# Kernel tuning notes

Measured on AMD Instinct MI355X. Metric: run time of the kernel, lower is better.

The kernel has to match this reference:

```python
import jax, jax.numpy as jnp
import numpy as np

B, D_IN, D_Z, D_H, D_T, D_REC = 8192, 1024, 256, 256, 16, 256


def _softplus_beta(x, beta):
    # torch F.softplus(x, beta) = (1/beta) * log(1 + exp(beta*x))
    return jax.nn.softplus(beta * x) / beta


def setup_inputs() -> dict:
    key = jax.random.key(0)
    ks = jax.random.split(key, 17)
    w = lambda k, o, i: jax.random.normal(k, (o, i), jnp.float32) * (1.0 / np.sqrt(i))
    return {
        "I_t": jax.random.uniform(ks[0], (B, D_IN), jnp.float32),
        "h_m_1": jax.random.uniform(ks[1], (B, D_H), jnp.float32),
        "z_m_1": jax.random.uniform(ks[2], (B, D_Z), jnp.float32),
        "theta_m_1": jax.random.normal(ks[3], (B, D_T), jnp.float32),
        "eps_z": jax.random.normal(ks[4], (B, D_Z), jnp.float32),
        "eps_zhat": jax.random.normal(ks[5], (B, D_Z), jnp.float32),
        "W_post_mu": w(ks[6], D_Z, D_IN),
        "W_post_lv": w(ks[7], D_Z, D_IN),
        "W_z2h": w(ks[8], D_H, D_Z),
        "W_h2h": w(ks[9], D_H, D_H),
        "W_prior_mu": w(ks[10], D_Z, D_H),
        "W_prior_lv": w(ks[11], D_Z, D_H),
        "W_i2t": w(ks[12], D_T, D_IN),
        "W_vip2t": w(ks[13], D_T, D_Z),
        "W_t2z": w(ks[14], D_Z, D_T),
        "W_rec1": w(ks[15], D_REC, D_Z),
        "W_rec2": w(ks[16], D_IN, D_REC),
    }


def reference(I_t, h_m_1, z_m_1, theta_m_1, eps_z, eps_zhat,
              W_post_mu, W_post_lv, W_z2h, W_h2h, W_prior_mu, W_prior_lv,
              W_i2t, W_vip2t, W_t2z, W_rec1, W_rec2):
    relu = jax.nn.relu
    # prior pathway (perception_only=True branch)
    mu_p = relu(h_m_1 @ W_prior_mu.T)                       # [B, D_Z]
    sigma_p = _softplus_beta(h_m_1 @ W_prior_lv.T, 1.2)     # [B, D_Z]
    # theta dynamics; vip_to_theta has Positive parametrization -> relu(W)
    theta_h = (0.5 * theta_m_1 + 0.1 * (I_t @ W_i2t.T)
               - jax.lax.stop_gradient(sigma_p) @ relu(W_vip2t).T)  # [B, D_T]
    theta = 0.001 * _softplus_beta(theta_h, 0.5)
    # posterior + reparameterized sample
    mu_q = relu(I_t @ W_post_mu.T)
    sigma_q = relu(I_t @ W_post_lv.T)
    raw_z = jnp.clip(mu_q + eps_z * sigma_q, 0.0, 1.0)
    thresholds = 10.0 * (theta @ relu(W_t2z).T)             # Positive parametrization
    z = relu(raw_z - thresholds)                            # [B, D_Z]
    # reconstruction (two bias-free linears + sigmoid)
    I_hat = jax.nn.sigmoid((z @ W_rec1.T) @ W_rec2.T)       # [B, D_IN]
    # higher-state update and prior sample
    h = relu(z_m_1 @ W_z2h.T + h_m_1 @ W_h2h.T)             # [B, D_H]
    z_hat = mu_p + eps_zhat * sigma_p                       # [B, D_Z]
    # losses (as in torch forward)
    spatial = jnp.mean((I_t - I_hat) ** 2)
    temporal = jnp.mean((jax.lax.stop_gradient(z) - z_hat) ** 2)
    energy = jnp.mean(jnp.abs(z))
    return (I_hat, z, h, z_hat, spatial, temporal, energy)
```

## Files before the change

### kernel.cpp

```cpp
#include <hip/hip_runtime.h>
#include <math.h>

#define BB 8192
#define DIN 1024
#define DZ 256
#define DH 256
#define DT 16
#define DREC 256

#define OFF_IHAT 0
#define OFF_Z    (BB * DIN)
#define OFF_H    (OFF_Z + BB * DZ)
#define OFF_ZHAT (OFF_H + BB * DH)
#define OFF_SCAL (OFF_ZHAT + BB * DZ)

#define WS_HBF   0
#define WS_ZM1   2097152
#define WS_W     4194304
#define W_PM  (WS_W + 0)
#define W_PL  (W_PM + 262144)
#define W_Z2H (W_PL + 262144)
#define W_H2H (W_Z2H + 65536)
#define W_PRM (W_H2H + 65536)
#define W_PRL (W_PRM + 65536)
#define W_I2T (W_PRL + 65536)
#define W_VIP (W_I2T + 16384)
#define W_R1  (W_VIP + 4096)
#define W_R2  (W_R1 + 65536)
#define WS_ENDW  (W_R2 + 262144)
#define WS_SIGMA WS_ENDW
#define WS_ZBF   (WS_SIGMA + 2097152)
#define WS_R1BF  (WS_ZBF + 2097152)

typedef unsigned short u16;
typedef __attribute__((ext_vector_type(8))) unsigned short u16x8;
typedef __attribute__((ext_vector_type(8))) __bf16 bf16x8;
typedef __attribute__((ext_vector_type(4))) float f32x4;

#define MFMA __builtin_amdgcn_mfma_f32_16x16x32_bf16

__device__ inline u16 f2bf(float f) {
  unsigned u = __builtin_bit_cast(unsigned, f);
  u += 0x7fff + ((u >> 16) & 1);
  return (u16)(u >> 16);
}
__device__ inline float softplus_stable(float y) {
  return (y > 20.f) ? y : log1pf(expf(y));
}
__device__ inline bf16x8 gf(const u16* p) {
  return __builtin_bit_cast(bf16x8, *(const u16x8*)p);
}
__device__ inline f32x4 fzero() { return (f32x4){0.f, 0.f, 0.f, 0.f}; }

__device__ inline float block_sum256(float v, float* rbuf) {
#pragma unroll
  for (int off = 32; off > 0; off >>= 1) v += __shfl_down(v, off, 64);
  __syncthreads();
  if ((threadIdx.x & 63) == 0) rbuf[threadIdx.x >> 6] = v;
  __syncthreads();
  return rbuf[0] + rbuf[1] + rbuf[2] + rbuf[3];
}

__device__ inline void dma64(u16* tile, const u16* __restrict__ gsrc,
                             int row0, int ldk, int k0) {
  const int lane = threadIdx.x & 63, w = threadIdx.x >> 6;
#pragma unroll
  for (int c = 0; c < 2; ++c) {
    int rb = w * 16 + c * 8;
    int r = rb + (lane >> 3);
    int gl = (lane & 7) ^ (r & 7);
    const u16* src = gsrc + (size_t)(row0 + r) * ldk + k0 + gl * 8;
    u16* dst = tile + rb * 64;
    __builtin_amdgcn_global_load_lds(
        (const __attribute__((address_space(1))) unsigned int*)(const void*)src,
        (__attribute__((address_space(3))) unsigned int*)(void*)dst, 16, 0, 0);
  }
}
__device__ inline void dma16(u16* tile, const u16* __restrict__ gsrc,
                             int ldk, int k0) {
  const int lane = threadIdx.x & 63, w = threadIdx.x >> 6;
  if (w < 2) {
    int rb = w * 8;
    int r = rb + (lane >> 3);
    int gl = (lane & 7) ^ (r & 7);
    const u16* src = gsrc + (size_t)r * ldk + k0 + gl * 8;
    u16* dst = tile + rb * 64;
    __builtin_amdgcn_global_load_lds(
        (const __attribute__((address_space(1))) unsigned int*)(const void*)src,
        (__attribute__((address_space(3))) unsigned int*)(void*)dst, 16, 0, 0);
  }
}
__device__ inline bf16x8 rd(const u16* tile, int r, int gl) {
  return gf(tile + r * 64 + ((gl ^ (r & 7)) * 8));
}

__global__ __launch_bounds__(256) void k_cvt(
    const float* __restrict__ I_t, const float* __restrict__ h_m_1,
    const float* __restrict__ z_m_1, const float* __restrict__ Wpm,
    const float* __restrict__ Wpl, const float* __restrict__ Wz2h,
    const float* __restrict__ Wh2h, const float* __restrict__ Wprm,
    const float* __restrict__ Wprl, const float* __restrict__ Wi2t,
    const float* __restrict__ Wv, const float* __restrict__ Wr1,
    const float* __restrict__ Wr2, u16* __restrict__ dstI,
    u16* __restrict__ dstW) {
  const int S1 = 8388608, S2 = 10485760, S3 = 12582912, S4 = 12845056,
            S5 = 13107200, S6 = 13172736, S7 = 13238272, S8 = 13303808,
            S9 = 13369344, S10 = 13385728, S11 = 13389824, S12 = 13455360,
            S13 = 13717504;
  int nchunk = S13 / 8;
  for (int c = blockIdx.x * 256 + threadIdx.x; c < nchunk;
       c += gridDim.x * 256) {
    int f = c * 8;
    const float* src;
    float scale = 1.f;
    bool nrelu = false;
    u16* dst;
    if (f < S1) {
      src = I_t + f;
      dst = dstI + f;
    } else {
      dst = dstW + (f - S1);
      if (f < S2)       src = h_m_1 + (f - S1);
      else if (f < S3)  src = z_m_1 + (f - S2);
      else if (f < S4)  src = Wpm + (f - S3);
      else if (f < S5)  src = Wpl + (f - S4);
      else if (f < S6)  src = Wz2h + (f - S5);
      else if (f < S7)  src = Wh2h + (f - S6);
      else if (f < S8)  src = Wprm + (f - S7);
      else if (f < S9)  src = Wprl + (f - S8);
      else if (f < S10) { src = Wi2t + (f - S9);  scale = 0.1f; }
      else if (f < S11) { src = Wv + (f - S10);   nrelu = true; }
      else if (f < S12) src = Wr1 + (f - S11);
      else              src = Wr2 + (f - S12);
    }
    float4 v0 = *(const float4*)(src);
    float4 v1 = *(const float4*)(src + 4);
    float vals[8] = {v0.x, v0.y, v0.z, v0.w, v1.x, v1.y, v1.z, v1.w};
    u16x8 o;
#pragma unroll
    for (int j = 0; j < 8; ++j) {
      float x = vals[j];
      x = nrelu ? -fmaxf(x, 0.f) : x * scale;
      o[j] = f2bf(x);
    }
    *(u16x8*)(dst) = o;
  }
}

__global__ __launch_bounds__(256, 4) void k_hp(
    const u16* __restrict__ h_bf, const u16* __restrict__ zm1,
    const u16* __restrict__ Wh2h, const u16* __restrict__ Wprm,
    const u16* __restrict__ Wprl, const u16* __restrict__ Wz2h,
    const float* __restrict__ eps_zhat, float* __restrict__ h_out,
    float* __restrict__ zhat_out, u16* __restrict__ sigma_bf) {
  __shared__ __align__(16) u16 As[64 * 64], B0s[64 * 64], B1s[64 * 64],
      B2s[64 * 64];
  const int tid = threadIdx.x, lane = tid & 63, w = tid >> 6;
  const int frow = lane & 15, fq = lane >> 4;
  const int col0 = blockIdx.x * 64, row0 = blockIdx.y * 64;
  f32x4 ah[4], am[4], as_[4];
#pragma unroll
  for (int i = 0; i < 4; ++i) { ah[i] = fzero(); am[i] = fzero(); as_[i] = fzero(); }

  for (int k0 = 0; k0 < DH; k0 += 64) {
    __syncthreads();
    dma64(As, h_bf, row0, DH, k0);
    dma64(B0s, Wh2h, col0, DH, k0);
    dma64(B1s, Wprm, col0, DH, k0);
    dma64(B2s, Wprl, col0, DH, k0);
    __syncthreads();
#pragma unroll
    for (int ks = 0; ks < 2; ++ks) {
      bf16x8 a = rd(As, w * 16 + frow, ks * 4 + fq);
#pragma unroll
      for (int ni = 0; ni < 4; ++ni) {
        ah[ni]  = MFMA(a, rd(B0s, ni * 16 + frow, ks * 4 + fq), ah[ni], 0, 0, 0);
        am[ni]  = MFMA(a, rd(B1s, ni * 16 + frow, ks * 4 + fq), am[ni], 0, 0, 0);
        as_[ni] = MFMA(a, rd(B2s, ni * 16 + frow, ks * 4 + fq), as_[ni], 0, 0, 0);
      }
    }
  }
  for (int k0 = 0; k0 < DZ; k0 += 64) {
    __syncthreads();
    dma64(As, zm1, row0, DZ, k0);
    dma64(B0s, Wz2h, col0, DZ, k0);
    __syncthreads();
#pragma unroll
    for (int ks = 0; ks < 2; ++ks) {
      bf16x8 a = rd(As, w * 16 + frow, ks * 4 + fq);
#pragma unroll
      for (int ni = 0; ni < 4; ++ni)
        ah[ni] = MFMA(a, rd(B0s, ni * 16 + frow, ks * 4 + fq), ah[ni], 0, 0, 0);
    }
  }
#pragma unroll
  for (int ni = 0; ni < 4; ++ni)
#pragma unroll
    for (int r = 0; r < 4; ++r) {
      int m = row0 + w * 16 + fq * 4 + r;
      int n = col0 + ni * 16 + frow;
      h_out[(size_t)m * DH + n] = fmaxf(ah[ni][r], 0.f);
      float sig = softplus_stable(1.2f * as_[ni][r]) * (1.f / 1.2f);
      float mu = fmaxf(am[ni][r], 0.f);
      zhat_out[(size_t)m * DZ + n] = mu + eps_zhat[(size_t)m * DZ + n] * sig;
      sigma_bf[(size_t)m * DZ + n] = f2bf(sig);
    }
}

__global__ __launch_bounds__(256, 4) void k_post(
    const u16* __restrict__ I_bf, const u16* __restrict__ Wpm,
    const u16* __restrict__ Wpl, const u16* __restrict__ Wi2t,
    const u16* __restrict__ Wv, const u16* __restrict__ sigma_bf,
    const float* __restrict__ theta_m_1, const float* __restrict__ W_t2z,
    const float* __restrict__ eps_z, const float* __restrict__ zhat,
    float* __restrict__ z_out, u16* __restrict__ z_bf,
    float* __restrict__ scal) {
  __shared__ __align__(16) u16 As[64 * 64], B0s[64 * 64], B1s[64 * 64],
      Bts[16 * 64];
  __shared__ float th_s[64 * 17];
  __shared__ float wt_s[64 * 17];
  __shared__ float rbuf[4];
  const int tid = threadIdx.x, lane = tid & 63, w = tid >> 6;
  const int frow = lane & 15, fq = lane >> 4;
  const int col0 = blockIdx.x * 64, row0 = blockIdx.y * 64;
  f32x4 accm[4], accs[4], acct = fzero();
#pragma unroll
  for (int i = 0; i < 4; ++i) { accm[i] = fzero(); accs[i] = fzero(); }

  for (int k0 = 0; k0 < DIN; k0 += 64) {
    __syncthreads();
    dma64(As, I_bf, row0, DIN, k0);
    dma64(B0s, Wpm, col0, DIN, k0);
    dma64(B1s, Wpl, col0, DIN, k0);
    dma16(Bts, Wi2t, DIN, k0);
    __syncthreads();
#pragma unroll
    for (int ks = 0; ks < 2; ++ks) {
      bf16x8 a = rd(As, w * 16 + frow, ks * 4 + fq);
#pragma unroll
      for (int ni = 0; ni < 4; ++ni) {
        accm[ni] = MFMA(a, rd(B0s, ni * 16 + frow, ks * 4 + fq), accm[ni], 0, 0, 0);
        accs[ni] = MFMA(a, rd(B1s, ni * 16 + frow, ks * 4 + fq), accs[ni], 0, 0, 0);
      }
      acct = MFMA(a, rd(Bts, frow, ks * 4 + fq), acct, 0, 0, 0);
    }
  }
  for (int k0 = 0; k0 < DZ; k0 += 64) {
    __syncthreads();
    dma64(As, sigma_bf, row0, DZ, k0);
    dma16(Bts, Wv, DZ, k0);
    __syncthreads();
#pragma unroll
    for (int ks = 0; ks < 2; ++ks)
      acct = MFMA(rd(As, w * 16 + frow, ks * 4 + fq),
                  rd(Bts, frow, ks * 4 + fq), acct, 0, 0, 0);
  }
  __syncthreads();
#pragma unroll
  for (int r = 0; r < 4; ++r) {
    int lr = w * 16 + fq * 4 + r;
    float th = 0.5f * theta_m_1[(size_t)(row0 + lr) * DT + frow] + acct[r];
    th_s[lr * 17 + frow] = 0.002f * softplus_stable(0.5f * th);
  }
  for (int idx = tid; idx < 64 * 16; idx += 256) {
    int n = idx >> 4, j = idx & 15;
    wt_s[n * 17 + j] = 10.f * fmaxf(W_t2z[(col0 + n) * DT + j], 0.f);
  }
  __syncthreads();
  float tsum = 0.f, esum = 0.f;
#pragma unroll
  for (int ni = 0; ni < 4; ++ni)
#pragma unroll
    for (int r = 0; r < 4; ++r) {
      int lr = w * 16 + fq * 4 + r;
      int ln = ni * 16 + frow;
      int m = row0 + lr;
      int n = col0 + ln;
      float mu = fmaxf(accm[ni][r], 0.f);
      float sq = fmaxf(accs[ni][r], 0.f);
      float raw = mu + eps_z[(size_t)m * DZ + n] * sq;
      raw = fminf(fmaxf(raw, 0.f), 1.f);
      float thr = 0.f;
#pragma unroll
      for (int j = 0; j < 16; ++j)
        thr = fmaf(th_s[lr * 17 + j], wt_s[ln * 17 + j], thr);
      float zz = fmaxf(raw - thr, 0.f);
      z_out[(size_t)m * DZ + n] = zz;
      z_bf[(size_t)m * DZ + n] = f2bf(zz);
      float d = zz - zhat[(size_t)m * DZ + n];
      tsum += d * d;
      esum += zz;
    }
  float t = block_sum256(tsum, rbuf);
  if (tid == 0) atomicAdd(scal + 1, t * (1.f / ((float)BB * DZ)));
  float e = block_sum256(esum, rbuf);
  if (tid == 0) atomicAdd(scal + 2, e * (1.f / ((float)BB * DZ)));
}

__global__ __launch_bounds__(256, 4) void k_rec1(const u16* __restrict__ z_bf,
                                                 const u16* __restrict__ Wr1,
                                                 u16* __restrict__ r1_bf) {
  __shared__ __align__(16) u16 As[64 * 64], B0s[64 * 64];
  const int tid = threadIdx.x, lane = tid & 63, w = tid >> 6;
  const int frow = lane & 15, fq = lane >> 4;
  const int col0 = blockIdx.x * 64, row0 = blockIdx.y * 64;
  f32x4 acc[4] = {fzero(), fzero(), fzero(), fzero()};
  for (int k0 = 0; k0 < DZ; k0 += 64) {
    __syncthreads();
    dma64(As, z_bf, row0, DZ, k0);
    dma64(B0s, Wr1, col0, DZ, k0);
    __syncthreads();
#pragma unroll
    for (int ks = 0; ks < 2; ++ks) {
      bf16x8 a = rd(As, w * 16 + frow, ks * 4 + fq);
#pragma unroll
      for (int ni = 0; ni < 4; ++ni)
        acc[ni] = MFMA(a, rd(B0s, ni * 16 + frow, ks * 4 + fq), acc[ni], 0, 0, 0);
    }
  }
#pragma unroll
  for (int ni = 0; ni < 4; ++ni)
#pragma unroll
    for (int r = 0; r < 4; ++r) {
      int m = row0 + w * 16 + fq * 4 + r;
      int n = col0 + ni * 16 + frow;
      r1_bf[(size_t)m * DREC + n] = f2bf(acc[ni][r]);
    }
}

__global__ __launch_bounds__(256, 4) void k_rec2(const u16* __restrict__ r1_bf,
                                                 const u16* __restrict__ Wr2,
                                                 const float* __restrict__ I_t,
                                                 float* __restrict__ ihat_out,
                                                 float* __restrict__ scal) {
  __shared__ __align__(16) u16 As[64 * 64], B0s[64 * 64];
  __shared__ float rbuf[4];
  const int tid = threadIdx.x, lane = tid & 63, w = tid >> 6;
  const int frow = lane & 15, fq = lane >> 4;
  const int col0 = blockIdx.x * 64, row0 = blockIdx.y * 64;
  f32x4 acc[4] = {fzero(), fzero(), fzero(), fzero()};
  for (int k0 = 0; k0 < DREC; k0 += 64) {
    __syncthreads();
    dma64(As, r1_bf, row0, DREC, k0);
    dma64(B0s, Wr2, col0, DREC, k0);
    __syncthreads();
#pragma unroll
    for (int ks = 0; ks < 2; ++ks) {
      bf16x8 a = rd(As, w * 16 + frow, ks * 4 + fq);
#pragma unroll
      for (int ni = 0; ni < 4; ++ni)
        acc[ni] = MFMA(a, rd(B0s, ni * 16 + frow, ks * 4 + fq), acc[ni], 0, 0, 0);
    }
  }
  float lsum = 0.f;
#pragma unroll
  for (int ni = 0; ni < 4; ++ni)
#pragma unroll
    for (int r = 0; r < 4; ++r) {
      int m = row0 + w * 16 + fq * 4 + r;
      int n = col0 + ni * 16 + frow;
      float ih = 1.f / (1.f + expf(-acc[ni][r]));
      ihat_out[(size_t)m * DIN + n] = ih;
      float d = I_t[(size_t)m * DIN + n] - ih;
      lsum += d * d;
    }
  float s = block_sum256(lsum, rbuf);
  if (tid == 0) atomicAdd(scal + 0, s * (1.f / ((float)BB * DIN)));
}

extern "C" void kernel_launch(void* const* d_in, const int* in_sizes, int n_in,
                              void* d_out, int out_size, void* d_ws,
                              size_t ws_size, hipStream_t stream) {
  const float* I_t       = (const float*)d_in[0];
  const float* h_m_1     = (const float*)d_in[1];
  const float* z_m_1     = (const float*)d_in[2];
  const float* theta_m_1 = (const float*)d_in[3];
  const float* eps_z     = (const float*)d_in[4];
  const float* eps_zhat  = (const float*)d_in[5];
  const float* W_post_mu = (const float*)d_in[6];
  const float* W_post_lv = (const float*)d_in[7];
  const float* W_z2h     = (const float*)d_in[8];
  const float* W_h2h     = (const float*)d_in[9];
  const float* W_prior_mu= (const float*)d_in[10];
  const float* W_prior_lv= (const float*)d_in[11];
  const float* W_i2t     = (const float*)d_in[12];
  const float* W_vip2t   = (const float*)d_in[13];
  const float* W_t2z     = (const float*)d_in[14];
  const float* W_rec1    = (const float*)d_in[15];
  const float* W_rec2    = (const float*)d_in[16];

  float* out = (float*)d_out;
  float* ihat = out + OFF_IHAT;
  float* zout = out + OFF_Z;
  float* hout = out + OFF_H;
  float* zhat = out + OFF_ZHAT;
  float* scal = out + OFF_SCAL;

  u16* ws_u = (u16*)d_ws;
  u16* I_bf = (u16*)ihat;
  u16* h_bf = ws_u + WS_HBF;
  u16* zm1_bf = ws_u + WS_ZM1;
  u16* sigma_bf = ws_u + WS_SIGMA;
  u16* z_bf = ws_u + WS_ZBF;
  u16* r1_bf = ws_u + WS_R1BF;

  hipMemsetAsync(scal, 0, 3 * sizeof(float), stream);

  k_cvt<<<2048, 256, 0, stream>>>(I_t, h_m_1, z_m_1, W_post_mu, W_post_lv,
                                  W_z2h, W_h2h, W_prior_mu, W_prior_lv, W_i2t,
                                  W_vip2t, W_rec1, W_rec2, I_bf, ws_u + WS_HBF);

  dim3 gz(DZ / 64, BB / 64);
  dim3 gi(DIN / 64, BB / 64);

  k_hp<<<gz, 256, 0, stream>>>(h_bf, zm1_bf, ws_u + W_H2H, ws_u + W_PRM,
                               ws_u + W_PRL, ws_u + W_Z2H, eps_zhat, hout,
                               zhat, sigma_bf);
  k_post<<<gz, 256, 0, stream>>>(I_bf, ws_u + W_PM, ws_u + W_PL, ws_u + W_I2T,
                                 ws_u + W_VIP, sigma_bf, theta_m_1, W_t2z,
                                 eps_z, zhat, zout, z_bf, scal);
  k_rec1<<<gz, 256, 0, stream>>>(z_bf, ws_u + W_R1, r1_bf);
  k_rec2<<<gi, 256, 0, stream>>>(r1_bf, ws_u + W_R2, I_t, ihat, scal);
}
```

Before: 273.7 us.

## Shrink row tiles, swizzle blocks across XCDs, and stage epilogues through LDS

The three DZ-wide GEMM kernels now use 32x64 tiles on a 1D grid of 1024 blocks, giving twice as many blocks and a 2x2 wave layout. Block IDs are remapped so consecutive XCDs take adjacent row blocks that share weight columns. All epilogues now write results to padded LDS and then emit coalesced float4 and u16x8 global stores and loads, replacing scattered per-element accesses. The trade-off is extra LDS round trips and barriers, plus less MFMA work per A-fragment load in the smaller tiles.

```diff
diff --git a/kernel.cpp b/kernel.cpp
--- a/kernel.cpp
+++ b/kernel.cpp
@@ -61,8 +61,26 @@
   return rbuf[0] + rbuf[1] + rbuf[2] + rbuf[3];
 }
 
-__device__ inline void dma64(u16* tile, const u16* __restrict__ gsrc,
-                             int row0, int ldk, int k0) {
+__device__ inline void decode4(int id, int rows, int& row0, int& col0) {
+  int xcd = id & 7, t = id >> 3;
+  col0 = (t & 3) * 64;
+  row0 = ((t >> 2) * 8 + xcd) * rows;
+}
+
+__device__ inline void dmaA32(u16* tile, const u16* __restrict__ gsrc,
+                              int row0, int ldk, int k0) {
+  const int lane = threadIdx.x & 63, w = threadIdx.x >> 6;
+  int rb = w * 8;
+  int r = rb + (lane >> 3);
+  int gl = (lane & 7) ^ (r & 7);
+  const u16* src = gsrc + (size_t)(row0 + r) * ldk + k0 + gl * 8;
+  u16* dst = tile + rb * 64;
+  __builtin_amdgcn_global_load_lds(
+      (const __attribute__((address_space(1))) unsigned int*)(const void*)src,
+      (__attribute__((address_space(3))) unsigned int*)(void*)dst, 16, 0, 0);
+}
+__device__ inline void dmaB64(u16* tile, const u16* __restrict__ gsrc,
+                              int row0, int ldk, int k0) {
   const int lane = threadIdx.x & 63, w = threadIdx.x >> 6;
 #pragma unroll
   for (int c = 0; c < 2; ++c) {
@@ -76,8 +94,8 @@
         (__attribute__((address_space(3))) unsigned int*)(void*)dst, 16, 0, 0);
   }
 }
-__device__ inline void dma16(u16* tile, const u16* __restrict__ gsrc,
-                             int ldk, int k0) {
+__device__ inline void dma16(u16* tile, const u16* __restrict__ gsrc, int ldk,
+                             int k0) {
   const int lane = threadIdx.x & 63, w = threadIdx.x >> 6;
   if (w < 2) {
     int rb = w * 8;
@@ -153,58 +171,97 @@
     const u16* __restrict__ Wprl, const u16* __restrict__ Wz2h,
     const float* __restrict__ eps_zhat, float* __restrict__ h_out,
     float* __restrict__ zhat_out, u16* __restrict__ sigma_bf) {
-  __shared__ __align__(16) u16 As[64 * 64], B0s[64 * 64], B1s[64 * 64],
-      B2s[64 * 64];
+  __shared__ __align__(16) u16 smem[2048 + 3 * 4096];
+  u16* As = smem;
+  u16* B0s = smem + 2048;
+  u16* B1s = B0s + 4096;
+  u16* B2s = B1s + 4096;
   const int tid = threadIdx.x, lane = tid & 63, w = tid >> 6;
   const int frow = lane & 15, fq = lane >> 4;
-  const int col0 = blockIdx.x * 64, row0 = blockIdx.y * 64;
-  f32x4 ah[4], am[4], as_[4];
-#pragma unroll
-  for (int i = 0; i < 4; ++i) { ah[i] = fzero(); am[i] = fzero(); as_[i] = fzero(); }
+  const int wr = w & 1, wc = w >> 1;
+  int row0, col0;
+  decode4(blockIdx.x, 32, row0, col0);
+
+  f32x4 ah[2], am[2], as_[2];
+#pragma unroll
+  for (int i = 0; i < 2; ++i) { ah[i] = fzero(); am[i] = fzero(); as_[i] = fzero(); }
 
   for (int k0 = 0; k0 < DH; k0 += 64) {
     __syncthreads();
-    dma64(As, h_bf, row0, DH, k0);
-    dma64(B0s, Wh2h, col0, DH, k0);
-    dma64(B1s, Wprm, col0, DH, k0);
-    dma64(B2s, Wprl, col0, DH, k0);
+    dmaA32(As, h_bf, row0, DH, k0);
+    dmaB64(B0s, Wh2h, col0, DH, k0);
+    dmaB64(B1s, Wprm, col0, DH, k0);
+    dmaB64(B2s, Wprl, col0, DH, k0);
     __syncthreads();
 #pragma unroll
     for (int ks = 0; ks < 2; ++ks) {
-      bf16x8 a = rd(As, w * 16 + frow, ks * 4 + fq);
-#pragma unroll
-      for (int ni = 0; ni < 4; ++ni) {
-        ah[ni]  = MFMA(a, rd(B0s, ni * 16 + frow, ks * 4 + fq), ah[ni], 0, 0, 0);
-        am[ni]  = MFMA(a, rd(B1s, ni * 16 + frow, ks * 4 + fq), am[ni], 0, 0, 0);
-        as_[ni] = MFMA(a, rd(B2s, ni * 16 + frow, ks * 4 + fq), as_[ni], 0, 0, 0);
+      bf16x8 a = rd(As, wr * 16 + frow, ks * 4 + fq);
+#pragma unroll
+      for (int ni = 0; ni < 2; ++ni) {
+        int br = wc * 32 + ni * 16 + frow;
+        ah[ni]  = MFMA(a, rd(B0s, br, ks * 4 + fq), ah[ni], 0, 0, 0);
+        am[ni]  = MFMA(a, rd(B1s, br, ks * 4 + fq), am[ni], 0, 0, 0);
+        as_[ni] = MFMA(a, rd(B2s, br, ks * 4 + fq), as_[ni], 0, 0, 0);
       }
     }
   }
   for (int k0 = 0; k0 < DZ; k0 += 64) {
     __syncthreads();
-    dma64(As, zm1, row0, DZ, k0);
-    dma64(B0s, Wz2h, col0, DZ, k0);
+    dmaA32(As, zm1, row0, DZ, k0);
+    dmaB64(B0s, Wz2h, col0, DZ, k0);
     __syncthreads();
 #pragma unroll
     for (int ks = 0; ks < 2; ++ks) {
-      bf16x8 a = rd(As, w * 16 + frow, ks * 4 + fq);
-#pragma unroll
-      for (int ni = 0; ni < 4; ++ni)
-        ah[ni] = MFMA(a, rd(B0s, ni * 16 + frow, ks * 4 + fq), ah[ni], 0, 0, 0);
-    }
-  }
-#pragma unroll
-  for (int ni = 0; ni < 4; ++ni)
+      bf16x8 a = rd(As, wr * 16 + frow, ks * 4 + fq);
+#pragma unroll
+      for (int ni = 0; ni < 2; ++ni)
+        ah[ni] = MFMA(a, rd(B0s, wc * 32 + ni * 16 + frow, ks * 4 + fq),
+                      ah[ni], 0, 0, 0);
+    }
+  }
+  __syncthreads();
+  float* ht = (float*)smem;
+  float* mt = (float*)(smem + 4224);
+  float* st = (float*)(smem + 8448);
+#pragma unroll
+  for (int ni = 0; ni < 2; ++ni)
 #pragma unroll
     for (int r = 0; r < 4; ++r) {
-      int m = row0 + w * 16 + fq * 4 + r;
-      int n = col0 + ni * 16 + frow;
-      h_out[(size_t)m * DH + n] = fmaxf(ah[ni][r], 0.f);
-      float sig = softplus_stable(1.2f * as_[ni][r]) * (1.f / 1.2f);
-      float mu = fmaxf(am[ni][r], 0.f);
-      zhat_out[(size_t)m * DZ + n] = mu + eps_zhat[(size_t)m * DZ + n] * sig;
-      sigma_bf[(size_t)m * DZ + n] = f2bf(sig);
-    }
+      int lr = wr * 16 + fq * 4 + r;
+      int ln = wc * 32 + ni * 16 + frow;
+      ht[lr * 66 + ln] = fmaxf(ah[ni][r], 0.f);
+      mt[lr * 66 + ln] = fmaxf(am[ni][r], 0.f);
+      st[lr * 66 + ln] = softplus_stable(1.2f * as_[ni][r]) * (1.f / 1.2f);
+    }
+  __syncthreads();
+  {
+    int lr2 = tid >> 3, c0 = (tid & 7) * 8;
+    int m2 = row0 + lr2;
+    float h8[8], mu8[8], sg8[8];
+#pragma unroll
+    for (int j = 0; j < 8; ++j) {
+      h8[j] = ht[lr2 * 66 + c0 + j];
+      mu8[j] = mt[lr2 * 66 + c0 + j];
+      sg8[j] = st[lr2 * 66 + c0 + j];
+    }
+    float* hp = h_out + (size_t)m2 * DH + col0 + c0;
+    *(float4*)hp = make_float4(h8[0], h8[1], h8[2], h8[3]);
+    *(float4*)(hp + 4) = make_float4(h8[4], h8[5], h8[6], h8[7]);
+    const float* ep = eps_zhat + (size_t)m2 * DZ + col0 + c0;
+    float4 e0 = ((const float4*)ep)[0], e1 = ((const float4*)ep)[1];
+    float e8[8] = {e0.x, e0.y, e0.z, e0.w, e1.x, e1.y, e1.z, e1.w};
+    float zh8[8];
+    u16x8 sb;
+#pragma unroll
+    for (int j = 0; j < 8; ++j) {
+      zh8[j] = mu8[j] + e8[j] * sg8[j];
+      sb[j] = f2bf(sg8[j]);
+    }
+    float* zp = zhat_out + (size_t)m2 * DZ + col0 + c0;
+    *(float4*)zp = make_float4(zh8[0], zh8[1], zh8[2], zh8[3]);
+    *(float4*)(zp + 4) = make_float4(zh8[4], zh8[5], zh8[6], zh8[7]);
+    *(u16x8*)(sigma_bf + (size_t)m2 * DZ + col0 + c0) = sb;
+  }
 }
 
 __global__ __launch_bounds__(256, 4) void k_post(
@@ -215,82 +272,110 @@
     const float* __restrict__ eps_z, const float* __restrict__ zhat,
     float* __restrict__ z_out, u16* __restrict__ z_bf,
     float* __restrict__ scal) {
-  __shared__ __align__(16) u16 As[64 * 64], B0s[64 * 64], B1s[64 * 64],
-      Bts[16 * 64];
-  __shared__ float th_s[64 * 17];
+  __shared__ __align__(16) u16 smem[2048 + 4096 + 4096 + 1024];
+  u16* As = smem;
+  u16* B0s = smem + 2048;
+  u16* B1s = B0s + 4096;
+  u16* Bts = B1s + 4096;
+  __shared__ float th_s[32 * 17];
   __shared__ float wt_s[64 * 17];
   __shared__ float rbuf[4];
   const int tid = threadIdx.x, lane = tid & 63, w = tid >> 6;
   const int frow = lane & 15, fq = lane >> 4;
-  const int col0 = blockIdx.x * 64, row0 = blockIdx.y * 64;
-  f32x4 accm[4], accs[4], acct = fzero();
-#pragma unroll
-  for (int i = 0; i < 4; ++i) { accm[i] = fzero(); accs[i] = fzero(); }
+  const int wr = w & 1, wc = w >> 1;
+  int row0, col0;
+  decode4(blockIdx.x, 32, row0, col0);
+
+  f32x4 accm[2], accs[2], acct = fzero();
+#pragma unroll
+  for (int i = 0; i < 2; ++i) { accm[i] = fzero(); accs[i] = fzero(); }
 
   for (int k0 = 0; k0 < DIN; k0 += 64) {
     __syncthreads();
-    dma64(As, I_bf, row0, DIN, k0);
-    dma64(B0s, Wpm, col0, DIN, k0);
-    dma64(B1s, Wpl, col0, DIN, k0);
+    dmaA32(As, I_bf, row0, DIN, k0);
+    dmaB64(B0s, Wpm, col0, DIN, k0);
+    dmaB64(B1s, Wpl, col0, DIN, k0);
     dma16(Bts, Wi2t, DIN, k0);
     __syncthreads();
 #pragma unroll
     for (int ks = 0; ks < 2; ++ks) {
-      bf16x8 a = rd(As, w * 16 + frow, ks * 4 + fq);
-#pragma unroll
-      for (int ni = 0; ni < 4; ++ni) {
-        accm[ni] = MFMA(a, rd(B0s, ni * 16 + frow, ks * 4 + fq), accm[ni], 0, 0, 0);
-        accs[ni] = MFMA(a, rd(B1s, ni * 16 + frow, ks * 4 + fq), accs[ni], 0, 0, 0);
+      bf16x8 a = rd(As, wr * 16 + frow, ks * 4 + fq);
+#pragma unroll
+      for (int ni = 0; ni < 2; ++ni) {
+        int br = wc * 32 + ni * 16 + frow;
+        accm[ni] = MFMA(a, rd(B0s, br, ks * 4 + fq), accm[ni], 0, 0, 0);
+        accs[ni] = MFMA(a, rd(B1s, br, ks * 4 + fq), accs[ni], 0, 0, 0);
       }
       acct = MFMA(a, rd(Bts, frow, ks * 4 + fq), acct, 0, 0, 0);
     }
   }
   for (int k0 = 0; k0 < DZ; k0 += 64) {
     __syncthreads();
-    dma64(As, sigma_bf, row0, DZ, k0);
+    dmaA32(As, sigma_bf, row0, DZ, k0);
     dma16(Bts, Wv, DZ, k0);
     __syncthreads();
 #pragma unroll
     for (int ks = 0; ks < 2; ++ks)
-      acct = MFMA(rd(As, w * 16 + frow, ks * 4 + fq),
+      acct = MFMA(rd(As, wr * 16 + frow, ks * 4 + fq),
                   rd(Bts, frow, ks * 4 + fq), acct, 0, 0, 0);
   }
   __syncthreads();
-#pragma unroll
-  for (int r = 0; r < 4; ++r) {
-    int lr = w * 16 + fq * 4 + r;
-    float th = 0.5f * theta_m_1[(size_t)(row0 + lr) * DT + frow] + acct[r];
-    th_s[lr * 17 + frow] = 0.002f * softplus_stable(0.5f * th);
+  if (wc == 0) {
+#pragma unroll
+    for (int r = 0; r < 4; ++r) {
+      int lr = wr * 16 + fq * 4 + r;
+      float th = 0.5f * theta_m_1[(size_t)(row0 + lr) * DT + frow] + acct[r];
+      th_s[lr * 17 + frow] = 0.002f * softplus_stable(0.5f * th);
+    }
   }
   for (int idx = tid; idx < 64 * 16; idx += 256) {
     int n = idx >> 4, j = idx & 15;
     wt_s[n * 17 + j] = 10.f * fmaxf(W_t2z[(col0 + n) * DT + j], 0.f);
   }
   __syncthreads();
-  float tsum = 0.f, esum = 0.f;
-#pragma unroll
-  for (int ni = 0; ni < 4; ++ni)
+  float* zt = (float*)B0s;
+#pragma unroll
+  for (int ni = 0; ni < 2; ++ni)
 #pragma unroll
     for (int r = 0; r < 4; ++r) {
-      int lr = w * 16 + fq * 4 + r;
-      int ln = ni * 16 + frow;
+      int lr = wr * 16 + fq * 4 + r;
+      int ln = wc * 32 + ni * 16 + frow;
       int m = row0 + lr;
-      int n = col0 + ln;
       float mu = fmaxf(accm[ni][r], 0.f);
       float sq = fmaxf(accs[ni][r], 0.f);
-      float raw = mu + eps_z[(size_t)m * DZ + n] * sq;
+      float raw = mu + eps_z[(size_t)m * DZ + col0 + ln] * sq;
       raw = fminf(fmaxf(raw, 0.f), 1.f);
       float thr = 0.f;
 #pragma unroll
       for (int j = 0; j < 16; ++j)
         thr = fmaf(th_s[lr * 17 + j], wt_s[ln * 17 + j], thr);
-      float zz = fmaxf(raw - thr, 0.f);
-      z_out[(size_t)m * DZ + n] = zz;
-      z_bf[(size_t)m * DZ + n] = f2bf(zz);
-      float d = zz - zhat[(size_t)m * DZ + n];
+      zt[lr * 66 + ln] = fmaxf(raw - thr, 0.f);
+    }
+  __syncthreads();
+  float tsum = 0.f, esum = 0.f;
+  {
+    int lr2 = tid >> 3, c0 = (tid & 7) * 8;
+    int m2 = row0 + lr2;
+    float z8[8];
+#pragma unroll
+    for (int j = 0; j < 8; ++j) z8[j] = zt[lr2 * 66 + c0 + j];
+    float* zp = z_out + (size_t)m2 * DZ + col0 + c0;
+    *(float4*)zp = make_float4(z8[0], z8[1], z8[2], z8[3]);
+    *(float4*)(zp + 4) = make_float4(z8[4], z8[5], z8[6], z8[7]);
+    u16x8 zb;
+#pragma unroll
+    for (int j = 0; j < 8; ++j) zb[j] = f2bf(z8[j]);
+    *(u16x8*)(z_bf + (size_t)m2 * DZ + col0 + c0) = zb;
+    const float* zhp = zhat + (size_t)m2 * DZ + col0 + c0;
+    float4 h0 = ((const float4*)zhp)[0], h1 = ((const float4*)zhp)[1];
+    float zh8[8] = {h0.x, h0.y, h0.z, h0.w, h1.x, h1.y, h1.z, h1.w};
+#pragma unroll
+    for (int j = 0; j < 8; ++j) {
+      float d = z8[j] - zh8[j];
       tsum += d * d;
-      esum += zz;
-    }
+      esum += z8[j];
+    }
+  }
   float t = block_sum256(tsum, rbuf);
   if (tid == 0) atomicAdd(scal + 1, t * (1.f / ((float)BB * DZ)));
   float e = block_sum256(esum, rbuf);
@@ -300,32 +385,48 @@
 __global__ __launch_bounds__(256, 4) void k_rec1(const u16* __restrict__ z_bf,
                                                  const u16* __restrict__ Wr1,
                                                  u16* __restrict__ r1_bf) {
-  __shared__ __align__(16) u16 As[64 * 64], B0s[64 * 64];
+  __shared__ __align__(16) u16 smem[2048 + 4096];
+  u16* As = smem;
+  u16* B0s = smem + 2048;
   const int tid = threadIdx.x, lane = tid & 63, w = tid >> 6;
   const int frow = lane & 15, fq = lane >> 4;
-  const int col0 = blockIdx.x * 64, row0 = blockIdx.y * 64;
-  f32x4 acc[4] = {fzero(), fzero(), fzero(), fzero()};
+  const int wr = w & 1, wc = w >> 1;
+  int row0, col0;
+  decode4(blockIdx.x, 32, row0, col0);
+  f32x4 acc[2] = {fzero(), fzero()};
   for (int k0 = 0; k0 < DZ; k0 += 64) {
     __syncthreads();
-    dma64(As, z_bf, row0, DZ, k0);
-    dma64(B0s, Wr1, col0, DZ, k0);
+    dmaA32(As, z_bf, row0, DZ, k0);
+    dmaB64(B0s, Wr1, col0, DZ, k0);
     __syncthreads();
 #pragma unroll
     for (int ks = 0; ks < 2; ++ks) {
-      bf16x8 a = rd(As, w * 16 + frow, ks * 4 + fq);
-#pragma unroll
-      for (int ni = 0; ni < 4; ++ni)
-        acc[ni] = MFMA(a, rd(B0s, ni * 16 + frow, ks * 4 + fq), acc[ni], 0, 0, 0);
-    }
-  }
-#pragma unroll
-  for (int ni = 0; ni < 4; ++ni)
+      bf16x8 a = rd(As, wr * 16 + frow, ks * 4 + fq);
+#pragma unroll
+      for (int ni = 0; ni < 2; ++ni)
+        acc[ni] = MFMA(a, rd(B0s, wc * 32 + ni * 16 + frow, ks * 4 + fq),
+                       acc[ni], 0, 0, 0);
+    }
+  }
+  __syncthreads();
+  float* rt = (float*)smem;
+#pragma unroll
+  for (int ni = 0; ni < 2; ++ni)
 #pragma unroll
     for (int r = 0; r < 4; ++r) {
-      int m = row0 + w * 16 + fq * 4 + r;
-      int n = col0 + ni * 16 + frow;
-      r1_bf[(size_t)m * DREC + n] = f2bf(acc[ni][r]);
-    }
+      int lr = wr * 16 + fq * 4 + r;
+      int ln = wc * 32 + ni * 16 + frow;
+      rt[lr * 66 + ln] = acc[ni][r];
+    }
+  __syncthreads();
+  {
+    int lr2 = tid >> 3, c0 = (tid & 7) * 8;
+    int m2 = row0 + lr2;
+    u16x8 rb;
+#pragma unroll
+    for (int j = 0; j < 8; ++j) rb[j] = f2bf(rt[lr2 * 66 + c0 + j]);
+    *(u16x8*)(r1_bf + (size_t)m2 * DREC + col0 + c0) = rb;
+  }
 }
 
 __global__ __launch_bounds__(256, 4) void k_rec2(const u16* __restrict__ r1_bf,
@@ -333,16 +434,24 @@
                                                  const float* __restrict__ I_t,
                                                  float* __restrict__ ihat_out,
                                                  float* __restrict__ scal) {
-  __shared__ __align__(16) u16 As[64 * 64], B0s[64 * 64];
+  __shared__ __align__(16) u16 smem[4096 + 4096];
+  u16* As = smem;
+  u16* B0s = smem + 4096;
   __shared__ float rbuf[4];
   const int tid = threadIdx.x, lane = tid & 63, w = tid >> 6;
   const int frow = lane & 15, fq = lane >> 4;
-  const int col0 = blockIdx.x * 64, row0 = blockIdx.y * 64;
+  int row0, col0;
+  {
+    int id = blockIdx.x;
+    int xcd = id & 7, t = id >> 3;
+    col0 = (t & 15) * 64;
+    row0 = ((t >> 4) * 8 + xcd) * 64;
+  }
   f32x4 acc[4] = {fzero(), fzero(), fzero(), fzero()};
   for (int k0 = 0; k0 < DREC; k0 += 64) {
     __syncthreads();
-    dma64(As, r1_bf, row0, DREC, k0);
-    dma64(B0s, Wr2, col0, DREC, k0);
+    dmaB64(As, r1_bf, row0, DREC, k0);
+    dmaB64(B0s, Wr2, col0, DREC, k0);
     __syncthreads();
 #pragma unroll
     for (int ks = 0; ks < 2; ++ks) {
@@ -353,17 +462,38 @@
     }
   }
   float lsum = 0.f;
-#pragma unroll
-  for (int ni = 0; ni < 4; ++ni)
-#pragma unroll
-    for (int r = 0; r < 4; ++r) {
-      int m = row0 + w * 16 + fq * 4 + r;
-      int n = col0 + ni * 16 + frow;
-      float ih = 1.f / (1.f + expf(-acc[ni][r]));
-      ihat_out[(size_t)m * DIN + n] = ih;
-      float d = I_t[(size_t)m * DIN + n] - ih;
+  float* it = (float*)smem;
+#pragma unroll 1
+  for (int p = 0; p < 2; ++p) {
+    __syncthreads();
+    if ((w >> 1) == p) {
+#pragma unroll
+      for (int ni = 0; ni < 4; ++ni)
+#pragma unroll
+        for (int r = 0; r < 4; ++r) {
+          int lrl = (w & 1) * 16 + fq * 4 + r;
+          int ln = ni * 16 + frow;
+          it[lrl * 66 + ln] = 1.f / (1.f + expf(-acc[ni][r]));
+        }
+    }
+    __syncthreads();
+    int lr2 = tid >> 3, c0 = (tid & 7) * 8;
+    int m2 = row0 + p * 32 + lr2;
+    float i8[8];
+#pragma unroll
+    for (int j = 0; j < 8; ++j) i8[j] = it[lr2 * 66 + c0 + j];
+    float* op = ihat_out + (size_t)m2 * DIN + col0 + c0;
+    *(float4*)op = make_float4(i8[0], i8[1], i8[2], i8[3]);
+    *(float4*)(op + 4) = make_float4(i8[4], i8[5], i8[6], i8[7]);
+    const float* ip = I_t + (size_t)m2 * DIN + col0 + c0;
+    float4 a0 = ((const float4*)ip)[0], a1 = ((const float4*)ip)[1];
+    float t8[8] = {a0.x, a0.y, a0.z, a0.w, a1.x, a1.y, a1.z, a1.w};
+#pragma unroll
+    for (int j = 0; j < 8; ++j) {
+      float d = t8[j] - i8[j];
       lsum += d * d;
     }
+  }
   float s = block_sum256(lsum, rbuf);
   if (tid == 0) atomicAdd(scal + 0, s * (1.f / ((float)BB * DIN)));
 }
@@ -410,15 +540,13 @@
                                   W_z2h, W_h2h, W_prior_mu, W_prior_lv, W_i2t,
                                   W_vip2t, W_rec1, W_rec2, I_bf, ws_u + WS_HBF);
 
-  dim3 gz(DZ / 64, BB / 64);
-  dim3 gi(DIN / 64, BB / 64);
-
-  k_hp<<<gz, 256, 0, stream>>>(h_bf, zm1_bf, ws_u + W_H2H, ws_u + W_PRM,
-                               ws_u + W_PRL, ws_u + W_Z2H, eps_zhat, hout,
-                               zhat, sigma_bf);
-  k_post<<<gz, 256, 0, stream>>>(I_bf, ws_u + W_PM, ws_u + W_PL, ws_u + W_I2T,
-                                 ws_u + W_VIP, sigma_bf, theta_m_1, W_t2z,
-                                 eps_z, zhat, zout, z_bf, scal);
-  k_rec1<<<gz, 256, 0, stream>>>(z_bf, ws_u + W_R1, r1_bf);
-  k_rec2<<<gi, 256, 0, stream>>>(r1_bf, ws_u + W_R2, I_t, ihat, scal);
-}
+  k_hp<<<1024, 256, 0, stream>>>(h_bf, zm1_bf, ws_u + W_H2H, ws_u + W_PRM,
+                                 ws_u + W_PRL, ws_u + W_Z2H, eps_zhat, hout,
+                                 zhat, sigma_bf);
+  k_post<<<1024, 256, 0, stream>>>(I_bf, ws_u + W_PM, ws_u + W_PL,
+                                   ws_u + W_I2T, ws_u + W_VIP, sigma_bf,
+                                   theta_m_1, W_t2z, eps_z, zhat, zout, z_bf,
+                                   scal);
+  k_rec1<<<1024, 256, 0, stream>>>(z_bf, ws_u + W_R1, r1_bf);
+  k_rec2<<<2048, 256, 0, stream>>>(r1_bf, ws_u + W_R2, I_t, ihat, scal);
+}
```

Result: faster. 245.7 us (-10.2%).
